# Optimization experiments

Measured on AMD Instinct MI355X. Metric: run time of the kernel, lower is better.

## Reference

```python
import jax, jax.numpy as jnp
import numpy as np

B, D_IN, H, T_EMB = 16384, 256, 512, 16


def _lin_params(key, out_dim, in_dim, bias):
    k1, k2 = jax.random.split(key)
    s = 1.0 / np.sqrt(in_dim)
    W = jax.random.uniform(k1, (out_dim, in_dim), jnp.float32, -s, s)
    b = jax.random.uniform(k2, (out_dim,), jnp.float32, -s, s) if bias else None
    return W, b


def setup_inputs() -> dict:
    key = jax.random.key(0)
    ks = jax.random.split(key, 20)
    x = jax.random.normal(ks[0], (B, D_IN), jnp.float32)
    h = jax.random.normal(ks[1], (B, H), jnp.float32)
    c_prev = jax.random.normal(ks[2], (B, H), jnp.float32)
    delt = jax.random.uniform(ks[3], (B, T_EMB), jnp.float32)

    W_ix, b_ix = _lin_params(ks[4], H, D_IN, True)
    W_ih, _ = _lin_params(ks[5], H, H, False)
    W_ic, _ = _lin_params(ks[6], H, H, False)
    W_fx, b_fx = _lin_params(ks[7], H, D_IN, True)
    W_fh, _ = _lin_params(ks[8], H, H, False)
    W_fc, _ = _lin_params(ks[9], H, H, False)
    W_tx, b_tx = _lin_params(ks[10], H, D_IN, True)
    W_tt, _ = _lin_params(ks[11], H, T_EMB, False)
    W_cx, b_cx = _lin_params(ks[12], H, D_IN, True)
    W_ch, _ = _lin_params(ks[13], H, H, False)
    W_ox, b_ox = _lin_params(ks[14], H, D_IN, True)
    W_oh, _ = _lin_params(ks[15], H, H, False)
    W_oc, _ = _lin_params(ks[16], H, H, False)
    W_ot, _ = _lin_params(ks[17], H, T_EMB, False)

    return dict(x=x, h=h, c_prev=c_prev, delt=delt,
                W_ix=W_ix, b_ix=b_ix, W_ih=W_ih, W_ic=W_ic,
                W_fx=W_fx, b_fx=b_fx, W_fh=W_fh, W_fc=W_fc,
                W_tx=W_tx, b_tx=b_tx, W_tt=W_tt,
                W_cx=W_cx, b_cx=b_cx, W_ch=W_ch,
                W_ox=W_ox, b_ox=b_ox, W_oh=W_oh, W_oc=W_oc, W_ot=W_ot)


def reference(x, h, c_prev, delt,
              W_ix, b_ix, W_ih, W_ic,
              W_fx, b_fx, W_fh, W_fc,
              W_tx, b_tx, W_tt,
              W_cx, b_cx, W_ch,
              W_ox, b_ox, W_oh, W_oc, W_ot):
    sig, tanh = jax.nn.sigmoid, jnp.tanh
    # input gate
    i = sig(x @ W_ix.T + b_ix + h @ W_ih.T + c_prev @ W_ic.T)
    # forget gate
    f = sig(x @ W_fx.T + b_fx + h @ W_fh.T + c_prev @ W_fc.T)
    # time gate: note inner sigmoid on the time-delta projection
    T = sig(x @ W_tx.T + b_tx + sig(delt @ W_tt.T))
    # candidate cell and new cell state
    k = tanh(x @ W_cx.T + b_cx + h @ W_ch.T)
    c_next = i * T * k + f * c_prev
    # output gate
    o = sig(x @ W_ox.T + b_ox + delt @ W_ot.T + h @ W_oh.T + c_prev @ W_oc.T)
    h_next = o * tanh(c_next)
    return (h_next, c_next, T)
```

## Files before the change

### kernel.cpp

```cpp
#include <hip/hip_runtime.h>
#include <cstdint>

#define B_SZ   16384
#define H_SZ   512
#define DIN    256
#define TEMB   16
#define KP     1344
#define KPB    1344
#define BH     8388608L
#define SLOT   16384
#define TSLOT  20480
#define GSTR   688128

typedef __attribute__((ext_vector_type(4))) float f32x4;
typedef __attribute__((ext_vector_type(4))) int   i32x4;

typedef const __attribute__((address_space(1))) unsigned int gu32_t;
typedef __attribute__((address_space(3)))       unsigned int lu32_t;

__device__ __forceinline__ void gld16(const void* g, void* l) {
  __builtin_amdgcn_global_load_lds((gu32_t*)(uintptr_t)g,
                                   (lu32_t*)(unsigned int)(uintptr_t)l, 16, 0, 0);
}

__device__ __forceinline__ float sigm(float v)  { return 1.0f / (1.0f + __expf(-v)); }
__device__ __forceinline__ float tanhx(float v) { return 2.0f / (1.0f + __expf(-2.0f * v)) - 1.0f; }

__device__ __forceinline__ signed char q8(float v, float inv) {
  int q = __float2int_rn(v * inv);
  q = (q > 127) ? 127 : (q < -127 ? -127 : q);
  return (signed char)q;
}

__global__ void prep_kernel(const float* __restrict__ x, const float* __restrict__ h,
                            const float* __restrict__ c, const float* __restrict__ dl,
                            const float* __restrict__ Wix, const float* __restrict__ Wih, const float* __restrict__ Wic,
                            const float* __restrict__ Wfx, const float* __restrict__ Wfh, const float* __restrict__ Wfc,
                            const float* __restrict__ Wtx, const float* __restrict__ Wtt,
                            const float* __restrict__ Wcx, const float* __restrict__ Wch,
                            const float* __restrict__ Wox, const float* __restrict__ Woh,
                            const float* __restrict__ Woc, const float* __restrict__ Wot,
                            signed char* __restrict__ Ap, float* __restrict__ sa,
                            signed char* __restrict__ Wp, float* __restrict__ sw) {
  __shared__ float row[KP];
  __shared__ float red[256];
  const int tid = threadIdx.x;
  if (blockIdx.x < 4096) {
    const int lane = tid & 63;
    const int m    = blockIdx.x * 4 + (tid >> 6);
    float4 v[6];
    float lmax = 0.f;
#pragma unroll
    for (int i = 0; i < 6; ++i) {
      const int k4 = (i * 64 + lane) * 4;
      float4 t = make_float4(0.f, 0.f, 0.f, 0.f);
      if (k4 < 256)       t = *(const float4*)(x  + (size_t)m * DIN  + k4);
      else if (k4 < 768)  t = *(const float4*)(h  + (size_t)m * H_SZ + (k4 - 256));
      else if (k4 < 1280) t = *(const float4*)(c  + (size_t)m * H_SZ + (k4 - 768));
      else if (k4 < 1296) t = *(const float4*)(dl + (size_t)m * TEMB + (k4 - 1280));
      v[i] = t;
      lmax = fmaxf(lmax, fmaxf(fmaxf(fabsf(t.x), fabsf(t.y)), fmaxf(fabsf(t.z), fabsf(t.w))));
    }
#pragma unroll
    for (int s = 1; s < 64; s <<= 1)
      lmax = fmaxf(lmax, __shfl_xor(lmax, s));
    const float smax = fmaxf(lmax, 1e-20f);
    const float inv  = 127.0f / smax;
    if (lane == 0) sa[m] = smax * (1.0f / 127.0f);
#pragma unroll
    for (int i = 0; i < 6; ++i) {
      const int k4 = (i * 64 + lane) * 4;
      if (k4 < KP) {
        char4 o;
        o.x = q8(v[i].x, inv); o.y = q8(v[i].y, inv);
        o.z = q8(v[i].z, inv); o.w = q8(v[i].w, inv);
        *(char4*)(Ap + (size_t)m * KPB + k4) = o;
      }
    }
    return;
  }
  const int R = blockIdx.x - 4096;
  const int g = R >> 9;
  const int n = R & 511;
  float lmax = 0.f;
  for (int i = tid; i < KP / 4; i += 256) {
    const int k4 = i * 4;
    const float* src = nullptr; long o = 0;
    if (g == 0) {
      if (k4 < 256)       { src = Wix; o = (long)n * 256 + k4; }
      else if (k4 < 768)  { src = Wih; o = (long)n * 512 + (k4 - 256); }
      else if (k4 < 1280) { src = Wic; o = (long)n * 512 + (k4 - 768); }
    } else if (g == 1) {
      if (k4 < 256)       { src = Wfx; o = (long)n * 256 + k4; }
      else if (k4 < 768)  { src = Wfh; o = (long)n * 512 + (k4 - 256); }
      else if (k4 < 1280) { src = Wfc; o = (long)n * 512 + (k4 - 768); }
    } else if (g == 2) {
      if (k4 < 256)       { src = Wtx; o = (long)n * 256 + k4; }
    } else if (g == 3) {
      if (k4 < 256)       { src = Wcx; o = (long)n * 256 + k4; }
      else if (k4 < 768)  { src = Wch; o = (long)n * 512 + (k4 - 256); }
    } else if (g == 4) {
      if (k4 < 256)       { src = Wox; o = (long)n * 256 + k4; }
      else if (k4 < 768)  { src = Woh; o = (long)n * 512 + (k4 - 256); }
      else if (k4 < 1280) { src = Woc; o = (long)n * 512 + (k4 - 768); }
      else if (k4 < 1296) { src = Wot; o = (long)n * 16 + (k4 - 1280); }
    } else {
      if (k4 >= 1280 && k4 < 1296) { src = Wtt; o = (long)n * 16 + (k4 - 1280); }
    }
    float4 v = make_float4(0.f, 0.f, 0.f, 0.f);
    if (src) v = *(const float4*)(src + o);
    *(float4*)(row + k4) = v;
    lmax = fmaxf(lmax, fmaxf(fmaxf(fabsf(v.x), fabsf(v.y)), fmaxf(fabsf(v.z), fabsf(v.w))));
  }
  red[tid] = lmax;
  __syncthreads();
  for (int s = 128; s > 0; s >>= 1) {
    if (tid < s) red[tid] = fmaxf(red[tid], red[tid + s]);
    __syncthreads();
  }
  const float smax = fmaxf(red[0], 1e-20f);
  const float inv  = 127.0f / smax;
  if (tid == 0) sw[R] = smax * (1.0f / 127.0f);
  for (int i = tid; i < KP / 4; i += 256) {
    const int k4 = i * 4;
    char4 o;
    o.x = q8(row[k4],     inv); o.y = q8(row[k4 + 1], inv);
    o.z = q8(row[k4 + 2], inv); o.w = q8(row[k4 + 3], inv);
    *(char4*)(Wp + (size_t)R * KPB + k4) = o;
  }
}


__device__ __forceinline__ void stageA(char* lds, int sb, int ht,
                                       const char* sAb, int wid) {
  const unsigned kb = (unsigned)ht * 64u;
  gld16(sAb + kb,             lds + sb + wid * 2048);
  gld16(sAb + kb + 16u * KPB, lds + sb + wid * 2048 + 1024);
}

template<unsigned CM, int NWE, bool ST>
__device__ __forceinline__ void phase(char* lds, int rs, int ws, int ht,
    const char* sAb, const char* wbase, int h, int wid, int aro, i32x4 acc[4][4]) {
  asm volatile("s_waitcnt vmcnt(%0)" :: "i"(NWE) : "memory");
  __builtin_amdgcn_s_barrier();
  __builtin_amdgcn_sched_barrier(0);
  const char* base = lds + rs;
  i32x4 a[4];
#pragma unroll
  for (int i = 0; i < 4; ++i)
    a[i] = *(const i32x4*)(base + aro + i * 1024);
  const size_t kb = (size_t)h * 64;
  i32x4 b[4];
  if (CM & 1u) b[0] = *(const i32x4*)(wbase + 0 * (size_t)GSTR + kb);
  if (CM & 2u) b[1] = *(const i32x4*)(wbase + 1 * (size_t)GSTR + kb);
  if (CM & 4u) b[2] = *(const i32x4*)(wbase + 3 * (size_t)GSTR + kb);
  if (CM & 8u) b[3] = *(const i32x4*)(wbase + 4 * (size_t)GSTR + kb);
  if (ST) stageA(lds, ws, ht, sAb, wid);
  __builtin_amdgcn_sched_barrier(0);
  __builtin_amdgcn_s_setprio(1);
#pragma unroll
  for (int r = 0; r < 4; ++r) {
    if (CM & (1u << r)) {
#pragma unroll
      for (int i = 0; i < 4; ++i)
        acc[r][i] = __builtin_amdgcn_mfma_i32_16x16x64_i8(a[i], b[r], acc[r][i], 0, 0, 0);
    }
  }
  __builtin_amdgcn_s_setprio(0);
}

__global__ __launch_bounds__(512, 4) void lstm_main(
    const signed char* __restrict__ Ap, const signed char* __restrict__ Wp,
    const float* __restrict__ sa, const float* __restrict__ sw,
    const float* __restrict__ c_prev,
    const float* __restrict__ b_ix, const float* __restrict__ b_fx,
    const float* __restrict__ b_cx, const float* __restrict__ b_ox,
    float* __restrict__ out)
{
  __shared__ __align__(16) char lds[3 * SLOT];

  const int tid  = threadIdx.x;
  const int lane = tid & 63;
  const int wid  = tid >> 6;

  const int bid = blockIdx.x;
  const int xcd = bid & 7;
  const int idx = bid >> 3;
  const int cb  = (xcd << 1) | (idx & 1);
  const int rb  = idx >> 1;
  const unsigned brow = (unsigned)rb * 256u;
  const int bcol = cb * 32;

  const int wr  = (wid >> 1) * 64;
  const int wcg = (wid & 1) * 16;
  const int lrow = lane & 15;
  const int kgrp = lane >> 4;

  i32x4 acc[4][4];
  {
    i32x4 z = {0, 0, 0, 0};
#pragma unroll
    for (int g = 0; g < 4; ++g)
#pragma unroll
      for (int i = 0; i < 4; ++i) acc[g][i] = z;
  }

  const int sread = ((kgrp + (lrow >> 1)) & 3) << 4;
  const int aro = (wr + lrow) * 64 + sread;

  const int l4 = lane >> 2;
  const int kslot = (((lane & 3) - ((lane >> 3) & 3)) & 3) << 4;
  const char* sAb   = (const char*)Ap + (size_t)(brow + wid * 32 + l4) * KPB + kslot;
  const char* wbase = (const char*)Wp + (size_t)(bcol + wcg + lrow) * KPB + kgrp * 16;

  stageA(lds, 0,    0, sAb, wid);
  stageA(lds, SLOT, 1, sAb, wid);

  int rs = 0;
#define PH(CMv, NWEv, STv, HT, H) do {                                         \
    int ws = (rs >= SLOT) ? rs - SLOT : rs + 2 * SLOT;                         \
    phase<CMv, NWEv, STv>(lds, rs, ws, HT, sAb, wbase, H, wid, aro, acc);      \
    rs = (rs == 2 * SLOT) ? 0 : rs + SLOT;                                     \
  } while (0)

#pragma unroll 1
  for (int h = 0; h < 12; ++h) PH(0xF, 2, true, h + 2, h);
#pragma unroll 1
  for (int h = 12; h < 19; ++h) PH(0xB, 2, true, h + 2, h);
  PH(0xB, 2, false, 0, 19);
  PH(0x8, 0, false, 0, 20);
#undef PH

  const float* Tvp = out + 2 * BH;
  const int n = bcol + wcg + lrow;
  const float bi = b_ix[n], bff = b_fx[n], bc = b_cx[n], bo = b_ox[n];
  const float s0 = sw[0 * 512 + n], s1 = sw[1 * 512 + n];
  const float s3 = sw[3 * 512 + n], s4 = sw[4 * 512 + n];
  const int rbase = kgrp * 4;
#pragma unroll
  for (int i = 0; i < 4; ++i) {
    const int m0 = (int)brow + wr + 16 * i + rbase;
    const float4 sa4 = *(const float4*)(sa + m0);
#pragma unroll
    for (int r = 0; r < 4; ++r) {
      const long m   = m0 + r;
      const long off = m * H_SZ + n;
      const float sr = (r == 0) ? sa4.x : (r == 1) ? sa4.y : (r == 2) ? sa4.z : sa4.w;
      const float iv = sigm((float)acc[0][i][r] * sr * s0 + bi);
      const float fv = sigm((float)acc[1][i][r] * sr * s1 + bff);
      const float kv = tanhx((float)acc[2][i][r] * sr * s3 + bc);
      const float ov = sigm((float)acc[3][i][r] * sr * s4 + bo);
      const float Tv = Tvp[off];
      const float cp = c_prev[off];
      const float cn = iv * Tv * kv + fv * cp;
      out[off]      = ov * tanhx(cn);
      out[BH + off] = cn;
    }
  }
}

template<unsigned SMASK>
__device__ __forceinline__ void stage_t(char* lds, int sb, int ht,
                                        const char* sAb, const char* sWb, int wid) {
  const unsigned kb = (unsigned)ht * 64u;
  gld16(sAb + kb,              lds + sb + wid * 2048);
  gld16(sAb + kb + 16u * KPB,  lds + sb + wid * 2048 + 1024);
  if (wid < 4) {
    const int r = wid >> 1, c = wid & 1;
    if (SMASK & (1u << r)) {
      const int g = (r == 0) ? 2 : 5;
      gld16(sWb + (unsigned)g * GSTR + (unsigned)c * (16u * KPB) + kb,
            lds + sb + 16384 + r * 2048 + c * 1024);
    }
  }
}

template<unsigned CM>
__device__ __forceinline__ void comp_t(const char* lds, int sb, int aro, int wro,
                                       i32x4 acc[2][4]) {
  const char* base = lds + sb;
  i32x4 a[4];
#pragma unroll
  for (int i = 0; i < 4; ++i)
    a[i] = *(const i32x4*)(base + aro + i * 1024);
#pragma unroll
  for (int r = 0; r < 2; ++r) {
    if (CM & (1u << r)) {
      i32x4 b = *(const i32x4*)(base + 16384 + r * 2048 + wro);
#pragma unroll
      for (int i = 0; i < 4; ++i)
        acc[r][i] = __builtin_amdgcn_mfma_i32_16x16x64_i8(a[i], b, acc[r][i], 0, 0, 0);
    }
  }
}

__global__ __launch_bounds__(512, 4) void tgate_kernel(
    const signed char* __restrict__ Ap, const signed char* __restrict__ Wp,
    const float* __restrict__ sa, const float* __restrict__ sw,
    const float* __restrict__ b_tx, float* __restrict__ out)
{
  __shared__ __align__(16) char lds[2 * TSLOT];

  const int tid  = threadIdx.x;
  const int lane = tid & 63;
  const int wid  = tid >> 6;

  const int bid = blockIdx.x;
  const int xcd = bid & 7;
  const int idx = bid >> 3;
  const int cb  = (xcd << 1) | (idx & 1);
  const int rb  = idx >> 1;
  const unsigned brow = (unsigned)rb * 256u;
  const int bcol = cb * 32;

  const int wr  = (wid >> 1) * 64;
  const int wcg = (wid & 1) * 16;
  const int lrow = lane & 15;
  const int kgrp = lane >> 4;

  i32x4 acc[2][4];
  {
    i32x4 z = {0, 0, 0, 0};
#pragma unroll
    for (int g = 0; g < 2; ++g)
#pragma unroll
      for (int i = 0; i < 4; ++i) acc[g][i] = z;
  }

  const int sread = ((kgrp + (lrow >> 1)) & 3) << 4;
  const int aro = (wr + lrow) * 64 + sread;
  const int wro = (wcg + lrow) * 64 + sread;

  const int l4 = lane >> 2;
  const int kslot = (((lane & 3) - ((lane >> 3) & 3)) & 3) << 4;
  const char* sAb = (const char*)Ap + (size_t)(brow + wid * 32 + l4) * KPB + kslot;
  const char* sWb = (const char*)Wp + (size_t)(bcol + l4) * KPB + kslot;

  stage_t<0x1>(lds, 0, 0, sAb, sWb, wid);
  __syncthreads();
  stage_t<0x1>(lds, TSLOT, 1, sAb, sWb, wid);
  comp_t<0x1>(lds, 0, aro, wro, acc);
  __syncthreads();
  stage_t<0x1>(lds, 0, 2, sAb, sWb, wid);
  comp_t<0x1>(lds, TSLOT, aro, wro, acc);
  __syncthreads();
  stage_t<0x1>(lds, TSLOT, 3, sAb, sWb, wid);
  comp_t<0x1>(lds, 0, aro, wro, acc);
  __syncthreads();
  stage_t<0x2>(lds, 0, 20, sAb, sWb, wid);
  comp_t<0x1>(lds, TSLOT, aro, wro, acc);
  __syncthreads();
  comp_t<0x2>(lds, 0, aro, wro, acc);

  const int n = bcol + wcg + lrow;
  const float bt = b_tx[n];
  const float s2 = sw[2 * 512 + n], s5 = sw[5 * 512 + n];
  const int rbase = kgrp * 4;
#pragma unroll
  for (int i = 0; i < 4; ++i) {
    const int m0 = (int)brow + wr + 16 * i + rbase;
    const float4 sa4 = *(const float4*)(sa + m0);
#pragma unroll
    for (int r = 0; r < 4; ++r) {
      const long off = (long)(m0 + r) * H_SZ + n;
      const float sr = (r == 0) ? sa4.x : (r == 1) ? sa4.y : (r == 2) ? sa4.z : sa4.w;
      const float inner = sigm((float)acc[1][i][r] * sr * s5);
      out[2 * BH + off] = sigm((float)acc[0][i][r] * sr * s2 + bt + inner);
    }
  }
}

extern "C" void kernel_launch(void* const* d_in, const int* in_sizes, int n_in,
                              void* d_out, int out_size, void* d_ws, size_t ws_size,
                              hipStream_t stream) {
  const float* x      = (const float*)d_in[0];
  const float* h      = (const float*)d_in[1];
  const float* c_prev = (const float*)d_in[2];
  const float* dl     = (const float*)d_in[3];
  const float* W_ix = (const float*)d_in[4];
  const float* b_ix = (const float*)d_in[5];
  const float* W_ih = (const float*)d_in[6];
  const float* W_ic = (const float*)d_in[7];
  const float* W_fx = (const float*)d_in[8];
  const float* b_fx = (const float*)d_in[9];
  const float* W_fh = (const float*)d_in[10];
  const float* W_fc = (const float*)d_in[11];
  const float* W_tx = (const float*)d_in[12];
  const float* b_tx = (const float*)d_in[13];
  const float* W_tt = (const float*)d_in[14];
  const float* W_cx = (const float*)d_in[15];
  const float* b_cx = (const float*)d_in[16];
  const float* W_ch = (const float*)d_in[17];
  const float* W_ox = (const float*)d_in[18];
  const float* b_ox = (const float*)d_in[19];
  const float* W_oh = (const float*)d_in[20];
  const float* W_oc = (const float*)d_in[21];
  const float* W_ot = (const float*)d_in[22];

  signed char* Ap8 = (signed char*)d_ws;
  signed char* Wp8 = (signed char*)d_ws + (size_t)B_SZ * KPB;
  float* sa = (float*)((char*)d_ws + (size_t)B_SZ * KPB + 6L * H_SZ * KPB);
  float* sw = sa + B_SZ;

  prep_kernel<<<4096 + 3072, 256, 0, stream>>>(
      x, h, c_prev, dl,
      W_ix, W_ih, W_ic, W_fx, W_fh, W_fc, W_tx, W_tt, W_cx, W_ch,
      W_ox, W_oh, W_oc, W_ot, Ap8, sa, Wp8, sw);

  tgate_kernel<<<1024, 512, 0, stream>>>(Ap8, Wp8, sa, sw, b_tx, (float*)d_out);

  lstm_main<<<1024, 512, 0, stream>>>(Ap8, Wp8, sa, sw, c_prev,
                                      b_ix, b_fx, b_cx, b_ox,
                                      (float*)d_out);
}
```

Measured before the change: 135.0 us.

## Fuse time-gate GEMM into main LSTM kernel and stage weights through LDS

Removes the separate tgate kernel launch. The time gate is now computed at the start of lstm_main, and its values are kept in LDS as packed bf16 so the epilogue no longer reloads them from global memory. The main K loop is restructured from a triple-buffered A-only LDS pipeline with direct global B loads into a double-buffered pipeline that stages both A and W tiles via global_load_lds with full __syncthreads per step. This saves a launch and a global read of T, but it uses bf16 T in the cell update, which slightly lowers precision, and the simpler pipeline may hide latency less well.

```diff
diff --git a/kernel.cpp b/kernel.cpp
--- a/kernel.cpp
+++ b/kernel.cpp
@@ -8,8 +8,8 @@
 #define KP     1344
 #define KPB    1344
 #define BH     8388608L
-#define SLOT   16384
-#define TSLOT  20480
+#define SLOT   24576
+#define TVOFF  49152
 #define GSTR   688128
 
 typedef __attribute__((ext_vector_type(4))) float f32x4;
@@ -30,6 +30,16 @@
   int q = __float2int_rn(v * inv);
   q = (q > 127) ? 127 : (q < -127 ? -127 : q);
   return (signed char)q;
+}
+
+__device__ __forceinline__ unsigned short f2bf(float f) {
+  unsigned int u = __float_as_uint(f);
+  u += 0x7FFFu + ((u >> 16) & 1u);
+  return (unsigned short)(u >> 16);
+}
+
+__device__ __forceinline__ float bf2f(unsigned short v) {
+  return __uint_as_float(((unsigned int)v) << 16);
 }
 
 __global__ void prep_kernel(const float* __restrict__ x, const float* __restrict__ h,
@@ -131,42 +141,65 @@
 }
 
 
-__device__ __forceinline__ void stageA(char* lds, int sb, int ht,
-                                       const char* sAb, int wid) {
+__device__ __forceinline__ void stage(char* lds, int sb, int ht,
+                                      const char* sAb, const char* sWb, int wid) {
   const unsigned kb = (unsigned)ht * 64u;
-  gld16(sAb + kb,             lds + sb + wid * 2048);
-  gld16(sAb + kb + 16u * KPB, lds + sb + wid * 2048 + 1024);
-}
-
-template<unsigned CM, int NWE, bool ST>
-__device__ __forceinline__ void phase(char* lds, int rs, int ws, int ht,
-    const char* sAb, const char* wbase, int h, int wid, int aro, i32x4 acc[4][4]) {
-  asm volatile("s_waitcnt vmcnt(%0)" :: "i"(NWE) : "memory");
-  __builtin_amdgcn_s_barrier();
-  __builtin_amdgcn_sched_barrier(0);
-  const char* base = lds + rs;
+  gld16(sAb + kb,              lds + sb + wid * 2048);
+  gld16(sAb + kb + 16u * KPB,  lds + sb + wid * 2048 + 1024);
+  const int r = wid >> 1, c = wid & 1;
+  const int g = r + (r >> 1);
+  gld16(sWb + (unsigned)g * GSTR + (unsigned)c * (16u * KPB) + kb,
+        lds + sb + 16384 + r * 2048 + c * 1024);
+}
+
+__device__ __forceinline__ void stage_tl(char* lds, int sb, int ht,
+                                         const char* sAb, const char* sWb, int wid) {
+  const unsigned kb = (unsigned)ht * 64u;
+  gld16(sAb + kb,              lds + sb + wid * 2048);
+  gld16(sAb + kb + 16u * KPB,  lds + sb + wid * 2048 + 1024);
+  if (wid < 4) {
+    const int r = wid >> 1, c = wid & 1;
+    const int g = (r == 0) ? 2 : 5;
+    gld16(sWb + (unsigned)g * GSTR + (unsigned)c * (16u * KPB) + kb,
+          lds + sb + 16384 + r * 2048 + c * 1024);
+  }
+}
+
+template<unsigned CM>
+__device__ __forceinline__ void comp(const char* lds, int sb, int aro, int wro,
+                                     i32x4 acc[4][4]) {
+  const char* base = lds + sb;
   i32x4 a[4];
 #pragma unroll
   for (int i = 0; i < 4; ++i)
     a[i] = *(const i32x4*)(base + aro + i * 1024);
-  const size_t kb = (size_t)h * 64;
-  i32x4 b[4];
-  if (CM & 1u) b[0] = *(const i32x4*)(wbase + 0 * (size_t)GSTR + kb);
-  if (CM & 2u) b[1] = *(const i32x4*)(wbase + 1 * (size_t)GSTR + kb);
-  if (CM & 4u) b[2] = *(const i32x4*)(wbase + 3 * (size_t)GSTR + kb);
-  if (CM & 8u) b[3] = *(const i32x4*)(wbase + 4 * (size_t)GSTR + kb);
-  if (ST) stageA(lds, ws, ht, sAb, wid);
-  __builtin_amdgcn_sched_barrier(0);
   __builtin_amdgcn_s_setprio(1);
 #pragma unroll
   for (int r = 0; r < 4; ++r) {
     if (CM & (1u << r)) {
+      i32x4 b = *(const i32x4*)(base + 16384 + r * 2048 + wro);
 #pragma unroll
       for (int i = 0; i < 4; ++i)
-        acc[r][i] = __builtin_amdgcn_mfma_i32_16x16x64_i8(a[i], b[r], acc[r][i], 0, 0, 0);
+        acc[r][i] = __builtin_amdgcn_mfma_i32_16x16x64_i8(a[i], b, acc[r][i], 0, 0, 0);
     }
   }
   __builtin_amdgcn_s_setprio(0);
+}
+
+__device__ __forceinline__ void comp_tl(const char* lds, int sb, int aro, int wro,
+                                        i32x4 acct[2][4]) {
+  const char* base = lds + sb;
+  i32x4 a[4];
+#pragma unroll
+  for (int i = 0; i < 4; ++i)
+    a[i] = *(const i32x4*)(base + aro + i * 1024);
+#pragma unroll
+  for (int r = 0; r < 2; ++r) {
+    i32x4 b = *(const i32x4*)(base + 16384 + r * 2048 + wro);
+#pragma unroll
+    for (int i = 0; i < 4; ++i)
+      acct[r][i] = __builtin_amdgcn_mfma_i32_16x16x64_i8(a[i], b, acct[r][i], 0, 0, 0);
+  }
 }
 
 __global__ __launch_bounds__(512, 4) void lstm_main(
@@ -174,10 +207,11 @@
     const float* __restrict__ sa, const float* __restrict__ sw,
     const float* __restrict__ c_prev,
     const float* __restrict__ b_ix, const float* __restrict__ b_fx,
+    const float* __restrict__ b_tx,
     const float* __restrict__ b_cx, const float* __restrict__ b_ox,
     float* __restrict__ out)
 {
-  __shared__ __align__(16) char lds[3 * SLOT];
+  __shared__ __align__(16) char lds[2 * SLOT + 16384];
 
   const int tid  = threadIdx.x;
   const int lane = tid & 63;
@@ -196,6 +230,68 @@
   const int lrow = lane & 15;
   const int kgrp = lane >> 4;
 
+  const int sread = ((kgrp + (lrow >> 1)) & 3) << 4;
+  const int aro = (wr + lrow) * 64 + sread;
+  const int wro = (wcg + lrow) * 64 + sread;
+
+  const int l4 = lane >> 2;
+  const int kslot = (((lane & 3) - ((lane >> 3) & 3)) & 3) << 4;
+  const char* sAb = (const char*)Ap + (size_t)(brow + wid * 32 + l4) * KPB + kslot;
+  const char* sWb = (const char*)Wp + (size_t)(bcol + l4) * KPB + kslot;
+
+  const int n = bcol + wcg + lrow;
+  const int rbase = kgrp * 4;
+
+  {
+    i32x4 acct[2][4];
+    {
+      i32x4 z = {0, 0, 0, 0};
+#pragma unroll
+      for (int r = 0; r < 2; ++r)
+#pragma unroll
+        for (int i = 0; i < 4; ++i) acct[r][i] = z;
+    }
+    stage_tl(lds, 0, 0, sAb, sWb, wid);
+    __syncthreads();
+    stage_tl(lds, SLOT, 1, sAb, sWb, wid);
+    comp_tl(lds, 0, aro, wro, acct);
+    __syncthreads();
+    stage_tl(lds, 0, 2, sAb, sWb, wid);
+    comp_tl(lds, SLOT, aro, wro, acct);
+    __syncthreads();
+    stage_tl(lds, SLOT, 3, sAb, sWb, wid);
+    comp_tl(lds, 0, aro, wro, acct);
+    __syncthreads();
+    stage_tl(lds, 0, 20, sAb, sWb, wid);
+    comp_tl(lds, SLOT, aro, wro, acct);
+    __syncthreads();
+    comp_tl(lds, 0, aro, wro, acct);
+
+    const float bt = b_tx[n];
+    const float s2 = sw[2 * 512 + n], s5 = sw[5 * 512 + n];
+    unsigned tvp[8];
+#pragma unroll
+    for (int w = 0; w < 8; ++w) tvp[w] = 0u;
+#pragma unroll
+    for (int i = 0; i < 4; ++i) {
+      const int m0 = (int)brow + wr + 16 * i + rbase;
+      const float4 sa4 = *(const float4*)(sa + m0);
+#pragma unroll
+      for (int r = 0; r < 4; ++r) {
+        const long off = (long)(m0 + r) * H_SZ + n;
+        const float sr = (r == 0) ? sa4.x : (r == 1) ? sa4.y : (r == 2) ? sa4.z : sa4.w;
+        const float inner = sigm((float)acct[1][i][r] * sr * s5);
+        const float tv = sigm((float)acct[0][i][r] * sr * s2 + bt + inner);
+        out[2 * BH + off] = tv;
+        const int ix = i * 4 + r;
+        tvp[ix >> 1] |= ((unsigned)f2bf(tv)) << ((ix & 1) * 16);
+      }
+    }
+    *(uint4*)(lds + TVOFF + tid * 32)      = make_uint4(tvp[0], tvp[1], tvp[2], tvp[3]);
+    *(uint4*)(lds + TVOFF + tid * 32 + 16) = make_uint4(tvp[4], tvp[5], tvp[6], tvp[7]);
+    __syncthreads();
+  }
+
   i32x4 acc[4][4];
   {
     i32x4 z = {0, 0, 0, 0};
@@ -205,38 +301,29 @@
       for (int i = 0; i < 4; ++i) acc[g][i] = z;
   }
 
-  const int sread = ((kgrp + (lrow >> 1)) & 3) << 4;
-  const int aro = (wr + lrow) * 64 + sread;
-
-  const int l4 = lane >> 2;
-  const int kslot = (((lane & 3) - ((lane >> 3) & 3)) & 3) << 4;
-  const char* sAb   = (const char*)Ap + (size_t)(brow + wid * 32 + l4) * KPB + kslot;
-  const char* wbase = (const char*)Wp + (size_t)(bcol + wcg + lrow) * KPB + kgrp * 16;
-
-  stageA(lds, 0,    0, sAb, wid);
-  stageA(lds, SLOT, 1, sAb, wid);
-
-  int rs = 0;
-#define PH(CMv, NWEv, STv, HT, H) do {                                         \
-    int ws = (rs >= SLOT) ? rs - SLOT : rs + 2 * SLOT;                         \
-    phase<CMv, NWEv, STv>(lds, rs, ws, HT, sAb, wbase, H, wid, aro, acc);      \
-    rs = (rs == 2 * SLOT) ? 0 : rs + SLOT;                                     \
-  } while (0)
-
+  stage(lds, 0, 0, sAb, sWb, wid);
+  __syncthreads();
 #pragma unroll 1
-  for (int h = 0; h < 12; ++h) PH(0xF, 2, true, h + 2, h);
+  for (int h = 0; h < 12; ++h) {
+    stage(lds, ((h + 1) & 1) * SLOT, h + 1, sAb, sWb, wid);
+    comp<0xF>(lds, (h & 1) * SLOT, aro, wro, acc);
+    __syncthreads();
+  }
 #pragma unroll 1
-  for (int h = 12; h < 19; ++h) PH(0xB, 2, true, h + 2, h);
-  PH(0xB, 2, false, 0, 19);
-  PH(0x8, 0, false, 0, 20);
-#undef PH
-
-  const float* Tvp = out + 2 * BH;
-  const int n = bcol + wcg + lrow;
+  for (int h = 12; h < 20; ++h) {
+    if (h < 20 - 1 + 1) {}
+    if (h + 1 <= 20) stage(lds, ((h + 1) & 1) * SLOT, h + 1, sAb, sWb, wid);
+    comp<0xB>(lds, (h & 1) * SLOT, aro, wro, acc);
+    __syncthreads();
+  }
+  comp<0x8>(lds, (20 & 1) * SLOT, aro, wro, acc);
+
   const float bi = b_ix[n], bff = b_fx[n], bc = b_cx[n], bo = b_ox[n];
   const float s0 = sw[0 * 512 + n], s1 = sw[1 * 512 + n];
   const float s3 = sw[3 * 512 + n], s4 = sw[4 * 512 + n];
-  const int rbase = kgrp * 4;
+  const uint4 tw0 = *(const uint4*)(lds + TVOFF + tid * 32);
+  const uint4 tw1 = *(const uint4*)(lds + TVOFF + tid * 32 + 16);
+  unsigned tvp[8] = {tw0.x, tw0.y, tw0.z, tw0.w, tw1.x, tw1.y, tw1.z, tw1.w};
 #pragma unroll
   for (int i = 0; i < 4; ++i) {
     const int m0 = (int)brow + wr + 16 * i + rbase;
@@ -250,122 +337,12 @@
       const float fv = sigm((float)acc[1][i][r] * sr * s1 + bff);
       const float kv = tanhx((float)acc[2][i][r] * sr * s3 + bc);
       const float ov = sigm((float)acc[3][i][r] * sr * s4 + bo);
-      const float Tv = Tvp[off];
+      const int ix = i * 4 + r;
+      const float Tv = bf2f((unsigned short)((tvp[ix >> 1] >> ((ix & 1) * 16)) & 0xFFFFu));
       const float cp = c_prev[off];
       const float cn = iv * Tv * kv + fv * cp;
       out[off]      = ov * tanhx(cn);
       out[BH + off] = cn;
-    }
-  }
-}
-
-template<unsigned SMASK>
-__device__ __forceinline__ void stage_t(char* lds, int sb, int ht,
-                                        const char* sAb, const char* sWb, int wid) {
-  const unsigned kb = (unsigned)ht * 64u;
-  gld16(sAb + kb,              lds + sb + wid * 2048);
-  gld16(sAb + kb + 16u * KPB,  lds + sb + wid * 2048 + 1024);
-  if (wid < 4) {
-    const int r = wid >> 1, c = wid & 1;
-    if (SMASK & (1u << r)) {
-      const int g = (r == 0) ? 2 : 5;
-      gld16(sWb + (unsigned)g * GSTR + (unsigned)c * (16u * KPB) + kb,
-            lds + sb + 16384 + r * 2048 + c * 1024);
-    }
-  }
-}
-
-template<unsigned CM>
-__device__ __forceinline__ void comp_t(const char* lds, int sb, int aro, int wro,
-                                       i32x4 acc[2][4]) {
-  const char* base = lds + sb;
-  i32x4 a[4];
-#pragma unroll
-  for (int i = 0; i < 4; ++i)
-    a[i] = *(const i32x4*)(base + aro + i * 1024);
-#pragma unroll
-  for (int r = 0; r < 2; ++r) {
-    if (CM & (1u << r)) {
-      i32x4 b = *(const i32x4*)(base + 16384 + r * 2048 + wro);
-#pragma unroll
-      for (int i = 0; i < 4; ++i)
-        acc[r][i] = __builtin_amdgcn_mfma_i32_16x16x64_i8(a[i], b, acc[r][i], 0, 0, 0);
-    }
-  }
-}
-
-__global__ __launch_bounds__(512, 4) void tgate_kernel(
-    const signed char* __restrict__ Ap, const signed char* __restrict__ Wp,
-    const float* __restrict__ sa, const float* __restrict__ sw,
-    const float* __restrict__ b_tx, float* __restrict__ out)
-{
-  __shared__ __align__(16) char lds[2 * TSLOT];
-
-  const int tid  = threadIdx.x;
-  const int lane = tid & 63;
-  const int wid  = tid >> 6;
-
-  const int bid = blockIdx.x;
-  const int xcd = bid & 7;
-  const int idx = bid >> 3;
-  const int cb  = (xcd << 1) | (idx & 1);
-  const int rb  = idx >> 1;
-  const unsigned brow = (unsigned)rb * 256u;
-  const int bcol = cb * 32;
-
-  const int wr  = (wid >> 1) * 64;
-  const int wcg = (wid & 1) * 16;
-  const int lrow = lane & 15;
-  const int kgrp = lane >> 4;
-
-  i32x4 acc[2][4];
-  {
-    i32x4 z = {0, 0, 0, 0};
-#pragma unroll
-    for (int g = 0; g < 2; ++g)
-#pragma unroll
-      for (int i = 0; i < 4; ++i) acc[g][i] = z;
-  }
-
-  const int sread = ((kgrp + (lrow >> 1)) & 3) << 4;
-  const int aro = (wr + lrow) * 64 + sread;
-  const int wro = (wcg + lrow) * 64 + sread;
-
-  const int l4 = lane >> 2;
-  const int kslot = (((lane & 3) - ((lane >> 3) & 3)) & 3) << 4;
-  const char* sAb = (const char*)Ap + (size_t)(brow + wid * 32 + l4) * KPB + kslot;
-  const char* sWb = (const char*)Wp + (size_t)(bcol + l4) * KPB + kslot;
-
-  stage_t<0x1>(lds, 0, 0, sAb, sWb, wid);
-  __syncthreads();
-  stage_t<0x1>(lds, TSLOT, 1, sAb, sWb, wid);
-  comp_t<0x1>(lds, 0, aro, wro, acc);
-  __syncthreads();
-  stage_t<0x1>(lds, 0, 2, sAb, sWb, wid);
-  comp_t<0x1>(lds, TSLOT, aro, wro, acc);
-  __syncthreads();
-  stage_t<0x1>(lds, TSLOT, 3, sAb, sWb, wid);
-  comp_t<0x1>(lds, 0, aro, wro, acc);
-  __syncthreads();
-  stage_t<0x2>(lds, 0, 20, sAb, sWb, wid);
-  comp_t<0x1>(lds, TSLOT, aro, wro, acc);
-  __syncthreads();
-  comp_t<0x2>(lds, 0, aro, wro, acc);
-
-  const int n = bcol + wcg + lrow;
-  const float bt = b_tx[n];
-  const float s2 = sw[2 * 512 + n], s5 = sw[5 * 512 + n];
-  const int rbase = kgrp * 4;
-#pragma unroll
-  for (int i = 0; i < 4; ++i) {
-    const int m0 = (int)brow + wr + 16 * i + rbase;
-    const float4 sa4 = *(const float4*)(sa + m0);
-#pragma unroll
-    for (int r = 0; r < 4; ++r) {
-      const long off = (long)(m0 + r) * H_SZ + n;
-      const float sr = (r == 0) ? sa4.x : (r == 1) ? sa4.y : (r == 2) ? sa4.z : sa4.w;
-      const float inner = sigm((float)acc[1][i][r] * sr * s5);
-      out[2 * BH + off] = sigm((float)acc[0][i][r] * sr * s2 + bt + inner);
     }
   }
 }
@@ -407,9 +384,7 @@
       W_ix, W_ih, W_ic, W_fx, W_fh, W_fc, W_tx, W_tt, W_cx, W_ch,
       W_ox, W_oh, W_oc, W_ot, Ap8, sa, Wp8, sw);
 
-  tgate_kernel<<<1024, 512, 0, stream>>>(Ap8, Wp8, sa, sw, b_tx, (float*)d_out);
-
   lstm_main<<<1024, 512, 0, stream>>>(Ap8, Wp8, sa, sw, c_prev,
-                                      b_ix, b_fx, b_cx, b_ox,
+                                      b_ix, b_fx, b_tx, b_cx, b_ox,
                                       (float*)d_out);
 }
```

Result: faster. 116.0 us (-14.0%).
